# Performance work log

Hardware: AMD Instinct MI355X
Metric: run time of the kernel (lower is better)

## Reference

```python
import jax, jax.numpy as jnp
import numpy as np
from jax import lax

B, S, D, K, H, NSLOT = 16, 128, 64, 64, 128, 96  # batch, seq/context, input, inter, hidden, slots


def setup_inputs() -> dict:
    key = jax.random.key(0)
    k = jax.random.split(key, 7)
    x_contexts = jax.random.normal(k[0], (B, S, D), jnp.float32)
    time_contexts = jax.random.randint(k[1], (B, S, S), 0, NSLOT + 1)
    dist_contexts = jax.random.randint(k[2], (B, S, S), 0, NSLOT + 1)
    context_masks = jax.random.randint(k[3], (B, S, S), 0, 2).astype(bool)
    # xavier-normal style init, matching nn.init.xavier_normal_ scales
    time_weights = jax.random.normal(k[4], (NSLOT + 1, D, K), jnp.float32) * (2.0 / (D + K)) ** 0.5
    dist_weights = jax.random.normal(k[5], (NSLOT + 1, K, H), jnp.float32) * (2.0 / (K + H)) ** 0.5
    hidden_weights = jax.random.normal(k[6], (H, H), jnp.float32) * (2.0 / (H + H)) ** 0.5
    return {"x_contexts": x_contexts, "time_contexts": time_contexts,
            "dist_contexts": dist_contexts, "context_masks": context_masks,
            "time_weights": time_weights, "dist_weights": dist_weights,
            "hidden_weights": hidden_weights}


def reference(x_contexts, time_contexts, dist_contexts, context_masks,
              time_weights, dist_weights, hidden_weights):
    # x_contexts: (B,S,D); *_contexts: (B,S,S) int; context_masks: (B,S,S) bool
    Bb, Ss, Dd = x_contexts.shape
    Hh = hidden_weights.shape[0]
    pos = jnp.arange(Ss)

    def step(h, xs):
        t_idx, d_idx, m, i = xs  # t_idx,d_idx,m: (B,S); i: step index
        # original slices context to :i+1; equivalent jit-friendly form: mask out j>i
        valid = m & (pos[None, :] <= i)  # (B,S)
        Tw = time_weights[t_idx]  # (B,S,D,K) gather
        Dw = dist_weights[d_idx]  # (B,S,K,H) gather
        # x @ (Tw @ Dw) reassociated as (x @ Tw) @ Dw to avoid (B,S,D,H) intermediate
        xt = jnp.einsum('bsd,bsdk->bsk', x_contexts, Tw)
        xc = jnp.einsum('bsk,bskh->bsh', xt, Dw)
        xc = jnp.where(valid[..., None], xc, 0.0).sum(axis=1)  # (B,H)
        h_new = jax.nn.sigmoid(xc + h @ hidden_weights)
        return h_new, h_new

    h0 = jnp.zeros((Bb, Hh), x_contexts.dtype)
    xs = (jnp.swapaxes(time_contexts, 0, 1),
          jnp.swapaxes(dist_contexts, 0, 1),
          jnp.swapaxes(context_masks, 0, 1),
          jnp.arange(Ss))
    hT, outs = lax.scan(step, h0, xs)
    # outputs: (B,S,H), final hidden with leading unsqueezed dim: (1,B,H)
    return jnp.swapaxes(outs, 0, 1), hT[None]
```

## Files before the change

kernel.cpp:

```cpp
#include <hip/hip_runtime.h>
#include <math.h>


#define B_ 16
#define S_ 128
#define D_ 64
#define K_ 64
#define H_ 128
#define NS 97
#define NB 128
#define MAXE 132096

#define XC_OFF 0
#define BH_T   262144
#define BH_D   (BH_T + NS * NB)
#define CNT_T  (BH_D + NS * NB)
#define CNT_D  (CNT_T + NS)
#define CNT_B  (CNT_D + NS)
#define OFF_T  (CNT_B + 2048)
#define OFF_D  (OFF_T + 98)
#define OFF_B  (OFF_D + 98)
#define ENT_T  291464
#define ENT_DX (ENT_T + MAXE)
#define ENT_DP (ENT_DX + MAXE)
#define XT16_OFF (ENT_DP + MAXE)
#define Y16_OFF  (XT16_OFF + MAXE * 32)
#define NEED_BYTES ((size_t)(Y16_OFF + (size_t)MAXE * 64) * 4)

typedef _Float16 h2_t __attribute__((ext_vector_type(2)));
typedef _Float16 f16x8 __attribute__((ext_vector_type(8)));
typedef float f32x4 __attribute__((ext_vector_type(4)));

#if __has_builtin(__builtin_amdgcn_fdot2)
#define FDOT2(a, b, c) __builtin_amdgcn_fdot2((a), (b), (c), false)
#else
#define FDOT2(a, b, c) ((c) + (float)(a)[0] * (float)(b)[0] + (float)(a)[1] * (float)(b)[1])
#endif


__global__ __launch_bounds__(256) void k_hist1(const int* __restrict__ tc,
                                               const int* __restrict__ dc,
                                               const int* __restrict__ mk,
                                               unsigned* wsi) {
    __shared__ unsigned ht[NS], hd[NS], hb[16];
    int tid = threadIdx.x, blk = blockIdx.x;
    if (tid < NS) { ht[tid] = 0; hd[tid] = 0; }
    if (tid < 16) hb[tid] = 0;
    __syncthreads();
    int base = blk * 2048;
    #pragma unroll
    for (int u = 0; u < 8; u++) {
        int idx = base + tid + u * 256;
        int i = (idx >> 7) & 127, j = idx & 127;
        if (j <= i && mk[idx] != 0) {
            atomicAdd(&ht[tc[idx]], 1u);
            atomicAdd(&hd[dc[idx]], 1u);
            atomicAdd(&hb[(idx >> 7) & 15], 1u);
        }
    }
    __syncthreads();
    if (tid < NS) {
        wsi[BH_T + tid * NB + blk] = ht[tid];
        wsi[BH_D + tid * NB + blk] = hd[tid];
    }
    if (tid < 16) wsi[CNT_B + blk * 16 + tid] = hb[tid];
}

template <int CH>
__device__ unsigned scan_region(unsigned* in, unsigned* out, int L, unsigned* s) {
    int tid = threadIdx.x;
    unsigned loc[CH], sum = 0;
    #pragma unroll
    for (int k = 0; k < CH; k++) {
        int idx = tid * CH + k;
        loc[k] = (idx < L) ? in[idx] : 0u;
        sum += loc[k];
    }
    s[tid] = sum;
    __syncthreads();
    for (int o = 1; o < 1024; o <<= 1) {
        unsigned a = (tid >= o) ? s[tid - o] : 0u;
        __syncthreads();
        s[tid] += a;
        __syncthreads();
    }
    unsigned total = s[1023];
    unsigned run = s[tid] - sum;
    __syncthreads();
    #pragma unroll
    for (int k = 0; k < CH; k++) {
        int idx = tid * CH + k;
        if (idx < L) { out[idx] = run; run += loc[k]; }
    }
    __syncthreads();
    return total;
}

__global__ __launch_bounds__(1024) void k_scan_all(unsigned* wsi) {
    __shared__ unsigned s[1024];
    int tid = threadIdx.x;

    unsigned tot = scan_region<25>(wsi + BH_T, wsi + BH_T, 2 * NS * NB, s);
    unsigned totT = wsi[BH_D];
    if (tid < NS) {
        unsigned b0 = wsi[BH_T + tid * NB];
        unsigned b1 = (tid < NS - 1) ? wsi[BH_T + (tid + 1) * NB] : totT;
        wsi[OFF_T + tid] = b0;
        wsi[CNT_T + tid] = b1 - b0;
        unsigned d0 = wsi[BH_D + tid * NB];
        unsigned d1 = (tid < NS - 1) ? wsi[BH_D + (tid + 1) * NB] : tot;
        wsi[OFF_D + tid] = d0 - totT;
        wsi[CNT_D + tid] = d1 - d0;
    }
    if (tid == 0) { wsi[OFF_T + NS] = totT; wsi[OFF_D + NS] = tot - totT; }
    __syncthreads();

    unsigned totB = scan_region<2>(wsi + CNT_B, wsi + OFF_B, 2048, s);
    if (tid == 0) wsi[OFF_B + 2048] = totB;
}

__global__ __launch_bounds__(256) void k_scatter(const int* __restrict__ tc,
                                                 const int* __restrict__ dc,
                                                 const int* __restrict__ mk,
                                                 unsigned* wsi, int useY) {
    __shared__ unsigned ct[NS], cd[NS], cb[16];
    int tid = threadIdx.x, blk = blockIdx.x;
    unsigned totT = wsi[OFF_T + NS];
    if (tid < NS) {
        ct[tid] = wsi[BH_T + tid * NB + blk];
        cd[tid] = wsi[BH_D + tid * NB + blk] - totT;
    }
    if (tid < 16) cb[tid] = wsi[OFF_B + blk * 16 + tid];
    __syncthreads();
    int base = blk * 2048;
    #pragma unroll
    for (int u = 0; u < 8; u++) {
        int idx = base + tid + u * 256;
        int i = (idx >> 7) & 127, j = idx & 127, b = idx >> 14;
        if (j <= i && mk[idx] != 0) {
            unsigned t = (unsigned)tc[idx], d = (unsigned)dc[idx];
            unsigned tpos = atomicAdd(&ct[t], 1u);
            wsi[ENT_T + tpos] = (unsigned)b | ((unsigned)i << 4) | ((unsigned)j << 11)
                              | (t << 18) | (d << 25);
            unsigned dpos = atomicAdd(&cd[d], 1u);
            unsigned yp = useY ? atomicAdd(&cb[(idx >> 7) & 15], 1u) : (unsigned)(idx >> 7);
            wsi[ENT_DX + dpos] = tpos;
            wsi[ENT_DP + dpos] = yp;
        }
    }
}

__global__ __launch_bounds__(256) void k_phaseA(const float* __restrict__ x,
                                                const float* __restrict__ tw,
                                                unsigned* wsi, float* wsf) {
    int t = blockIdx.x, c = blockIdx.y;
    int rows = (int)wsi[CNT_T + t] - c * 128;
    if (rows <= 0) return;
    if (rows > 128) rows = 128;
    unsigned base = wsi[OFF_T + t] + c * 128;

    __shared__ float stw[4096];
    __shared__ float sx[8192];
    __shared__ unsigned ent[128];
    int tid = threadIdx.x;

    const float4* twg = (const float4*)(tw + t * 4096);
    float4* stw4 = (float4*)stw;
    #pragma unroll
    for (int q = 0; q < 4; q++) stw4[q * 256 + tid] = twg[q * 256 + tid];
    if (tid < 128) ent[tid] = (tid < rows) ? wsi[ENT_T + base + tid] : 0u;
    __syncthreads();

    int lane16 = tid & 15, rquot = tid >> 4;
    #pragma unroll
    for (int p = 0; p < 8; p++) {
        int r = p * 16 + rquot;
        float4 v = make_float4(0.f, 0.f, 0.f, 0.f);
        if (r < rows) {
            unsigned e = ent[r];
            int b = e & 15, j = (e >> 11) & 127;
            v = *(const float4*)(x + (b * S_ + j) * D_ + lane16 * 4);
        }
        int col4 = lane16 ^ (r & 15);
        float* dst = &sx[r * 64 + col4 * 4];
        dst[0] = v.x; dst[1] = v.y; dst[2] = v.z; dst[3] = v.w;
    }
    __syncthreads();

    int rgrp = tid & 15, cgrp = tid >> 4;
    float4 acc[8];
    #pragma unroll
    for (int i = 0; i < 8; i++) acc[i] = make_float4(0.f, 0.f, 0.f, 0.f);
    #pragma unroll 4
    for (int dd = 0; dd < 64; dd++) {
        float4 w = stw4[dd * 16 + cgrp];
        int s_idx = (((dd >> 2) ^ rgrp) << 2) + (dd & 3);
        #pragma unroll
        for (int i = 0; i < 8; i++) {
            float a = sx[(rgrp + 16 * i) * 64 + s_idx];
            acc[i].x += a * w.x; acc[i].y += a * w.y;
            acc[i].z += a * w.z; acc[i].w += a * w.w;
        }
    }
    _Float16* XT = (_Float16*)(wsf + XT16_OFF);
    #pragma unroll
    for (int i = 0; i < 8; i++) {
        int r = rgrp + 16 * i;
        if (r < rows) {
            union { _Float16 h[4]; double d64; } u;
            u.h[0] = (_Float16)acc[i].x; u.h[1] = (_Float16)acc[i].y;
            u.h[2] = (_Float16)acc[i].z; u.h[3] = (_Float16)acc[i].w;
            *(double*)&XT[(size_t)(base + r) * 64 + cgrp * 4] = u.d64;
        }
    }
}

__global__ __launch_bounds__(256) void k_phaseB(const float* __restrict__ dw,
                                                unsigned* wsi, float* wsf, int useY) {
    int d = blockIdx.x, c = blockIdx.y;
    int rows = (int)wsi[CNT_D + d] - c * 128;
    if (rows <= 0) return;
    if (rows > 128) rows = 128;
    unsigned base = wsi[OFF_D + d] + c * 128;

    __shared__ _Float16 sa[128 * 64];
    __shared__ _Float16 sb[64 * 128];
    __shared__ unsigned entx_s[128], entp_s[128];
    int tid = threadIdx.x;

    if (tid < 128) {
        entx_s[tid] = (tid < rows) ? wsi[ENT_DX + base + tid] : 0u;
        entp_s[tid] = (tid < rows) ? wsi[ENT_DP + base + tid] : 0u;
    }
    const float4* dwg = (const float4*)(dw + (size_t)d * 8192);
    #pragma unroll
    for (int q = 0; q < 8; q++) {
        float4 v = dwg[q * 256 + tid];
        union { _Float16 h[4]; double d64; } u;
        u.h[0] = (_Float16)v.x; u.h[1] = (_Float16)v.y;
        u.h[2] = (_Float16)v.z; u.h[3] = (_Float16)v.w;
        *(double*)&sb[(q * 256 + tid) * 4] = u.d64;
    }
    __syncthreads();

    {
        int r = tid >> 1, hh = tid & 1;
        const _Float16* XT = (const _Float16*)(wsf + XT16_OFF);
        const f16x8* src = (const f16x8*)(XT + (size_t)entx_s[r] * 64 + hh * 32);
        #pragma unroll
        for (int mm = 0; mm < 4; mm++) {
            f16x8 hv = {0, 0, 0, 0, 0, 0, 0, 0};
            if (r < rows) hv = src[mm];
            int chunk = hh * 4 + mm;
            *(f16x8*)&sa[r * 64 + (chunk ^ (r & 7)) * 8] = hv;
        }
    }
    __syncthreads();

    int w = tid >> 6, lane = tid & 63;
    int l15 = lane & 15, lg = lane >> 4;
    f16x8 bf[2][2];
    #pragma unroll
    for (int n = 0; n < 2; n++) {
        int col = w * 32 + n * 16 + l15;
        #pragma unroll
        for (int ks = 0; ks < 2; ks++) {
            int kb = ks * 32 + lg * 8;
            f16x8 t;
            #pragma unroll
            for (int e = 0; e < 8; e++) t[e] = sb[(kb + e) * 128 + col];
            bf[n][ks] = t;
        }
    }
    f32x4 acc[8][2];
    f32x4 z = {0.f, 0.f, 0.f, 0.f};
    #pragma unroll
    for (int m = 0; m < 8; m++) { acc[m][0] = z; acc[m][1] = z; }

    #pragma unroll
    for (int m = 0; m < 8; m++) {
        int row = m * 16 + l15;
        f16x8 a0 = *(f16x8*)&sa[row * 64 + ((lg) ^ (row & 7)) * 8];
        f16x8 a1 = *(f16x8*)&sa[row * 64 + ((4 + lg) ^ (row & 7)) * 8];
        #pragma unroll
        for (int n = 0; n < 2; n++) {
            acc[m][n] = __builtin_amdgcn_mfma_f32_16x16x32_f16(a0, bf[n][0], acc[m][n], 0, 0, 0);
            acc[m][n] = __builtin_amdgcn_mfma_f32_16x16x32_f16(a1, bf[n][1], acc[m][n], 0, 0, 0);
        }
    }

    if (useY) {
        _Float16* Y16 = (_Float16*)(wsf + Y16_OFF);
        #pragma unroll
        for (int m = 0; m < 8; m++) {
            #pragma unroll
            for (int reg = 0; reg < 4; reg++) {
                int row = m * 16 + lg * 4 + reg;
                if (row < rows) {
                    _Float16* p = Y16 + (size_t)entp_s[row] * 128 + w * 32 + l15;
                    p[0]  = (_Float16)acc[m][0][reg];
                    p[16] = (_Float16)acc[m][1][reg];
                }
            }
        }
    } else {
        float* XC = wsf + XC_OFF;
        #pragma unroll
        for (int m = 0; m < 8; m++) {
            #pragma unroll
            for (int reg = 0; reg < 4; reg++) {
                int row = m * 16 + lg * 4 + reg;
                if (row < rows) {
                    float* p = XC + (size_t)entp_s[row] * 128 + w * 32 + l15;
                    atomicAdd(p + 0,  acc[m][0][reg]);
                    atomicAdd(p + 16, acc[m][1][reg]);
                }
            }
        }
    }
}

__global__ __launch_bounds__(128) void k_reduce(unsigned* wsi, float* wsf) {
    int bi = blockIdx.x, tid = threadIdx.x;
    unsigned n = wsi[CNT_B + bi], off = wsi[OFF_B + bi];
    const _Float16* Yp = (const _Float16*)(wsf + Y16_OFF) + (size_t)off * 128 + tid;
    float a0 = 0.f, a1 = 0.f, a2 = 0.f, a3 = 0.f;
    unsigned e = 0;
    for (; e + 4 <= n; e += 4) {
        a0 += (float)Yp[(size_t)e * 128];
        a1 += (float)Yp[(size_t)(e + 1) * 128];
        a2 += (float)Yp[(size_t)(e + 2) * 128];
        a3 += (float)Yp[(size_t)(e + 3) * 128];
    }
    for (; e < n; e++) a0 += (float)Yp[(size_t)e * 128];
    wsf[XC_OFF + (size_t)bi * 128 + tid] = (a0 + a1) + (a2 + a3);
}

#define RSTEP(XCREG, IDX, CURB)                                                \
    {                                                                          \
        float xc_use = XCREG;                                                  \
        if (i + 4 + (IDX) < 128) XCREG = XC[(i + 4 + (IDX)) * 128];            \
        const float4* hb = (const float4*)&h16[CURB][0];                       \
        float a0 = 0.f, a1 = 0.f, a2 = 0.f, a3 = 0.f;                          \
        _Pragma("unroll")                                                      \
        for (int q = 0; q < 16; q++) {                                         \
            union { float4 f4; h2_t h2[4]; } u;                                \
            u.f4 = hb[q];                                                      \
            a0 = FDOT2(u.h2[0], w2[4 * q + 0], a0);                            \
            a1 = FDOT2(u.h2[1], w2[4 * q + 1], a1);                            \
            a2 = FDOT2(u.h2[2], w2[4 * q + 2], a2);                            \
            a3 = FDOT2(u.h2[3], w2[4 * q + 3], a3);                            \
        }                                                                      \
        float v = xc_use + (a0 + a1) + (a2 + a3);                              \
        v = 1.f / (1.f + __expf(-v));                                          \
        val = v;                                                               \
        ((_Float16*)&h16[(CURB) ^ 1][0])[col] = (_Float16)v;                   \
        out[(size_t)(b * 128 + i + (IDX)) * 128 + col] = v;                    \
        __syncthreads();                                                       \
    }

__global__ __launch_bounds__(128) void k_recur(const float* __restrict__ hw,
                                               const float* __restrict__ wsf,
                                               float* __restrict__ out) {
    int b = blockIdx.x;
    __shared__ h2_t h16[2][64];
    int tid = threadIdx.x;
    int lane = tid & 63, wv = tid >> 6;
    int col = wv * 64 + lane;

    h2_t w2[64];
    #pragma unroll
    for (int m = 0; m < 64; m++) {
        h2_t p;
        p[0] = (_Float16)hw[(2 * m) * 128 + col];
        p[1] = (_Float16)hw[(2 * m + 1) * 128 + col];
        w2[m] = p;
    }
    if (tid < 64) h16[0][tid] = (h2_t)(_Float16)0.f;
    __syncthreads();

    const float* XC = wsf + XC_OFF + (size_t)b * 128 * 128 + col;
    float xc0 = XC[0 * 128], xc1 = XC[1 * 128], xc2 = XC[2 * 128], xc3 = XC[3 * 128];
    float val = 0.f;
    for (int i = 0; i < 128; i += 4) {
        RSTEP(xc0, 0, 0)
        RSTEP(xc1, 1, 1)
        RSTEP(xc2, 2, 0)
        RSTEP(xc3, 3, 1)
    }
    out[(size_t)B_ * S_ * H_ + b * 128 + col] = val;
}

extern "C" void kernel_launch(void* const* d_in, const int* in_sizes, int n_in,
                              void* d_out, int out_size, void* d_ws, size_t ws_size,
                              hipStream_t stream) {
    const float* x  = (const float*)d_in[0];
    const int*   tc = (const int*)d_in[1];
    const int*   dc = (const int*)d_in[2];
    const int*   mk = (const int*)d_in[3];
    const float* tw = (const float*)d_in[4];
    const float* dw = (const float*)d_in[5];
    const float* hw = (const float*)d_in[6];
    float*    out = (float*)d_out;
    float*    wsf = (float*)d_ws;
    unsigned* wsi = (unsigned*)d_ws;
    char*     wsb = (char*)d_ws;

    int useY = (ws_size >= NEED_BYTES) ? 1 : 0;
    if (!useY)
        hipMemsetAsync(wsb, 0, (size_t)262144 * 4, stream);

    k_hist1<<<dim3(NB), dim3(256), 0, stream>>>(tc, dc, mk, wsi);
    k_scan_all<<<dim3(1), dim3(1024), 0, stream>>>(wsi);
    k_scatter<<<dim3(NB), dim3(256), 0, stream>>>(tc, dc, mk, wsi, useY);
    k_phaseA<<<dim3(NS, 16), dim3(256), 0, stream>>>(x, tw, wsi, wsf);
    k_phaseB<<<dim3(NS, 16), dim3(256), 0, stream>>>(dw, wsi, wsf, useY);
    if (useY) k_reduce<<<dim3(2048), dim3(128), 0, stream>>>(wsi, wsf);
    k_recur<<<dim3(16), dim3(128), 0, stream>>>(hw, wsf, out);
}
```

Before: 134.5 us.

## Run recurrence for all batches in one block using MFMA 16x16x32 f16

Replaces the per-batch recurrence (16 blocks of 128 threads doing fdot2 matvecs) with a single 512-thread block that treats all 16 batch rows as a 16x128 matrix. Each step is now a 16x128x128 matmul issued as four MFMA 16x16x32 f16 instructions per wave. Hidden weights are staged through shared memory as fp16 fragments, and the hidden state is double-buffered in padded LDS. This aims to cut the serial per-step latency of the 128-step loop, at the cost of running on a single CU with a 512-thread barrier every step.

```diff
diff --git a/kernel.cpp b/kernel.cpp
--- a/kernel.cpp
+++ b/kernel.cpp
@@ -27,15 +27,8 @@
 #define Y16_OFF  (XT16_OFF + MAXE * 32)
 #define NEED_BYTES ((size_t)(Y16_OFF + (size_t)MAXE * 64) * 4)
 
-typedef _Float16 h2_t __attribute__((ext_vector_type(2)));
 typedef _Float16 f16x8 __attribute__((ext_vector_type(8)));
 typedef float f32x4 __attribute__((ext_vector_type(4)));
-
-#if __has_builtin(__builtin_amdgcn_fdot2)
-#define FDOT2(a, b, c) __builtin_amdgcn_fdot2((a), (b), (c), false)
-#else
-#define FDOT2(a, b, c) ((c) + (float)(a)[0] * (float)(b)[0] + (float)(a)[1] * (float)(b)[1])
-#endif
 
 
 __global__ __launch_bounds__(256) void k_hist1(const int* __restrict__ tc,
@@ -336,59 +329,89 @@
     wsf[XC_OFF + (size_t)bi * 128 + tid] = (a0 + a1) + (a2 + a3);
 }
 
-#define RSTEP(XCREG, IDX, CURB)                                                \
+#define LD_XC(V, I)                                                            \
+    { V.x = XCp[0 * 16384 + (I) * 128]; V.y = XCp[1 * 16384 + (I) * 128];      \
+      V.z = XCp[2 * 16384 + (I) * 128]; V.w = XCp[3 * 16384 + (I) * 128]; }
+
+#define QSTEP(XCR, IDX, CUR)                                                   \
     {                                                                          \
-        float xc_use = XCREG;                                                  \
-        if (i + 4 + (IDX) < 128) XCREG = XC[(i + 4 + (IDX)) * 128];            \
-        const float4* hb = (const float4*)&h16[CURB][0];                       \
-        float a0 = 0.f, a1 = 0.f, a2 = 0.f, a3 = 0.f;                          \
-        _Pragma("unroll")                                                      \
-        for (int q = 0; q < 16; q++) {                                         \
-            union { float4 f4; h2_t h2[4]; } u;                                \
-            u.f4 = hb[q];                                                      \
-            a0 = FDOT2(u.h2[0], w2[4 * q + 0], a0);                            \
-            a1 = FDOT2(u.h2[1], w2[4 * q + 1], a1);                            \
-            a2 = FDOT2(u.h2[2], w2[4 * q + 2], a2);                            \
-            a3 = FDOT2(u.h2[3], w2[4 * q + 3], a3);                            \
-        }                                                                      \
-        float v = xc_use + (a0 + a1) + (a2 + a3);                              \
-        v = 1.f / (1.f + __expf(-v));                                          \
-        val = v;                                                               \
-        ((_Float16*)&h16[(CURB) ^ 1][0])[col] = (_Float16)v;                   \
-        out[(size_t)(b * 128 + i + (IDX)) * 128 + col] = v;                    \
+        const _Float16* hbp = &hbuf[CUR][(size_t)l15 * 136];                   \
+        f16x8 a0 = *(const f16x8*)&hbp[lg * 8];                                \
+        f16x8 a1 = *(const f16x8*)&hbp[32 + lg * 8];                           \
+        f16x8 a2 = *(const f16x8*)&hbp[64 + lg * 8];                           \
+        f16x8 a3 = *(const f16x8*)&hbp[96 + lg * 8];                           \
+        f32x4 acc = {0.f, 0.f, 0.f, 0.f};                                      \
+        acc = __builtin_amdgcn_mfma_f32_16x16x32_f16(a0, bf[0], acc, 0, 0, 0); \
+        acc = __builtin_amdgcn_mfma_f32_16x16x32_f16(a1, bf[1], acc, 0, 0, 0); \
+        acc = __builtin_amdgcn_mfma_f32_16x16x32_f16(a2, bf[2], acc, 0, 0, 0); \
+        acc = __builtin_amdgcn_mfma_f32_16x16x32_f16(a3, bf[3], acc, 0, 0, 0); \
+        float4 xcu = XCR;                                                      \
+        if (i + 4 + (IDX) < 128) LD_XC(XCR, i + 4 + (IDX));                    \
+        float v0 = 1.f / (1.f + __expf(-(xcu.x + acc[0])));                    \
+        float v1 = 1.f / (1.f + __expf(-(xcu.y + acc[1])));                    \
+        float v2 = 1.f / (1.f + __expf(-(xcu.z + acc[2])));                    \
+        float v3 = 1.f / (1.f + __expf(-(xcu.w + acc[3])));                    \
+        _Float16* hn = &hbuf[(CUR) ^ 1][0];                                    \
+        hn[(lg * 4 + 0) * 136 + col] = (_Float16)v0;                           \
+        hn[(lg * 4 + 1) * 136 + col] = (_Float16)v1;                           \
+        hn[(lg * 4 + 2) * 136 + col] = (_Float16)v2;                           \
+        hn[(lg * 4 + 3) * 136 + col] = (_Float16)v3;                           \
+        float* op = out + (size_t)(i + (IDX)) * 128 + col;                     \
+        op[(size_t)(lg * 4 + 0) * 16384] = v0;                                 \
+        op[(size_t)(lg * 4 + 1) * 16384] = v1;                                 \
+        op[(size_t)(lg * 4 + 2) * 16384] = v2;                                 \
+        op[(size_t)(lg * 4 + 3) * 16384] = v3;                                 \
+        lastv = make_float4(v0, v1, v2, v3);                                   \
         __syncthreads();                                                       \
     }
 
-__global__ __launch_bounds__(128) void k_recur(const float* __restrict__ hw,
+__global__ __launch_bounds__(512) void k_recur(const float* __restrict__ hw,
                                                const float* __restrict__ wsf,
                                                float* __restrict__ out) {
-    int b = blockIdx.x;
-    __shared__ h2_t h16[2][64];
+    __shared__ _Float16 sb[128 * 128];
+    __shared__ _Float16 hbuf[2][16 * 136];
     int tid = threadIdx.x;
-    int lane = tid & 63, wv = tid >> 6;
-    int col = wv * 64 + lane;
-
-    h2_t w2[64];
-    #pragma unroll
-    for (int m = 0; m < 64; m++) {
-        h2_t p;
-        p[0] = (_Float16)hw[(2 * m) * 128 + col];
-        p[1] = (_Float16)hw[(2 * m + 1) * 128 + col];
-        w2[m] = p;
-    }
-    if (tid < 64) h16[0][tid] = (h2_t)(_Float16)0.f;
-    __syncthreads();
-
-    const float* XC = wsf + XC_OFF + (size_t)b * 128 * 128 + col;
-    float xc0 = XC[0 * 128], xc1 = XC[1 * 128], xc2 = XC[2 * 128], xc3 = XC[3 * 128];
-    float val = 0.f;
+    int wv = tid >> 6, lane = tid & 63;
+    int l15 = lane & 15, lg = lane >> 4;
+    int col = wv * 16 + l15;
+
+    const float4* hwg = (const float4*)hw;
+    #pragma unroll
+    for (int q = 0; q < 8; q++) {
+        float4 v = hwg[q * 512 + tid];
+        union { _Float16 h[4]; double d64; } u;
+        u.h[0] = (_Float16)v.x; u.h[1] = (_Float16)v.y;
+        u.h[2] = (_Float16)v.z; u.h[3] = (_Float16)v.w;
+        *(double*)&sb[(q * 512 + tid) * 4] = u.d64;
+    }
+    for (int q = tid; q < 16 * 136 / 2; q += 512) ((unsigned*)&hbuf[0][0])[q] = 0u;
+    __syncthreads();
+
+    f16x8 bf[4];
+    #pragma unroll
+    for (int ks = 0; ks < 4; ks++) {
+        f16x8 t;
+        #pragma unroll
+        for (int e = 0; e < 8; e++) t[e] = sb[(ks * 32 + lg * 8 + e) * 128 + col];
+        bf[ks] = t;
+    }
+
+    const float* XCp = wsf + XC_OFF + (size_t)(lg * 4) * 16384 + col;
+    float4 xc0, xc1, xc2, xc3;
+    LD_XC(xc0, 0) LD_XC(xc1, 1) LD_XC(xc2, 2) LD_XC(xc3, 3)
+    float4 lastv = make_float4(0.f, 0.f, 0.f, 0.f);
+
     for (int i = 0; i < 128; i += 4) {
-        RSTEP(xc0, 0, 0)
-        RSTEP(xc1, 1, 1)
-        RSTEP(xc2, 2, 0)
-        RSTEP(xc3, 3, 1)
-    }
-    out[(size_t)B_ * S_ * H_ + b * 128 + col] = val;
+        QSTEP(xc0, 0, 0)
+        QSTEP(xc1, 1, 1)
+        QSTEP(xc2, 2, 0)
+        QSTEP(xc3, 3, 1)
+    }
+    float* fp = out + (size_t)B_ * S_ * H_ + col;
+    fp[(lg * 4 + 0) * 128] = lastv.x;
+    fp[(lg * 4 + 1) * 128] = lastv.y;
+    fp[(lg * 4 + 2) * 128] = lastv.z;
+    fp[(lg * 4 + 3) * 128] = lastv.w;
 }
 
 extern "C" void kernel_launch(void* const* d_in, const int* in_sizes, int n_in,
@@ -416,5 +439,5 @@
     k_phaseA<<<dim3(NS, 16), dim3(256), 0, stream>>>(x, tw, wsi, wsf);
     k_phaseB<<<dim3(NS, 16), dim3(256), 0, stream>>>(dw, wsi, wsf, useY);
     if (useY) k_reduce<<<dim3(2048), dim3(128), 0, stream>>>(wsi, wsf);
-    k_recur<<<dim3(16), dim3(128), 0, stream>>>(hw, wsf, out);
-}
+    k_recur<<<dim3(1), dim3(512), 0, stream>>>(hw, wsf, out);
+}
```

Result: slower. 162.8 us (+21.1%).
